# Optimization experiments

Measured on AMD Instinct MI355X. Metric: run time of the kernel, lower is better.

The kernel has to match this reference:

```python
import jax, jax.numpy as jnp
import numpy as np

B, CIN, H, W = 4, 256, 32, 32
COUT, DK, DV, NH = 256, 64, 64, 8
L = H * W
DKH = DK // NH
DVH = DV // NH
ALPHA, BETA = 0.5, 0.5
PAD = 1
LEAK = 0.01
GN_EPS = 1e-5


def conv2d(x, w, b=None, padding=0):
    out = jax.lax.conv_general_dilated(
        x, w, window_strides=(1, 1),
        padding=[(padding, padding), (padding, padding)],
        dimension_numbers=('NCHW', 'OIHW', 'NCHW'))
    if b is not None:
        out = out + b[None, :, None, None]
    return out


def rel_to_abs(x):
    # x: [B, Nh, L, 2L-1] -> [B, Nh, L, L]
    b, nh, l, _ = x.shape
    x = jnp.concatenate([x, jnp.zeros((b, nh, l, 1), x.dtype)], axis=3)
    flat = x.reshape(b, nh, l * 2 * l)
    flat = jnp.concatenate([flat, jnp.zeros((b, nh, l - 1), x.dtype)], axis=2)
    final = flat.reshape(b, nh, l + 1, 2 * l - 1)
    return final[:, :, :l, l - 1:]


def setup_inputs() -> dict:
    key = jax.random.key(0)
    ks = jax.random.split(key, 8)
    s = 0.02
    return {
        'x': jax.random.normal(ks[0], (B, CIN, H, W), jnp.float32),
        'prev_att': jax.random.normal(ks[1], (B, NH, L, L), jnp.float32) * 0.1,
        'conv_v': jax.random.normal(ks[2], (COUT - DV, CIN, 3, 3), jnp.float32) * s,
        'conv_g': jnp.ones((COUT - DV, 1, 1, 1), jnp.float32),
        'conv_b': jnp.zeros((COUT - DV,), jnp.float32),
        'qkv_w': jax.random.normal(ks[3], (2 * DK + DV, CIN, 1, 1), jnp.float32) * s,
        'qkv_b': jnp.zeros((2 * DK + DV,), jnp.float32),
        'attc_w': jax.random.normal(ks[4], (NH, NH, 3, 3), jnp.float32) * s,
        'attc_b': jnp.zeros((NH,), jnp.float32),
        'gn_w': jnp.ones((NH,), jnp.float32),
        'gn_b': jnp.zeros((NH,), jnp.float32),
        'rel_k': jax.random.normal(ks[5], (2 * L - 1, DKH), jnp.float32),
    }


def reference(x, prev_att, conv_v, conv_g, conv_b, qkv_w, qkv_b,
              attc_w, attc_b, gn_w, gn_b, rel_k):
    # ---- weight-normed conv branch (k < 1) ----
    vnorm = jnp.sqrt(jnp.sum(conv_v * conv_v, axis=(1, 2, 3), keepdims=True))
    w_eff = conv_g * conv_v / vnorm
    conv_out = conv2d(x, w_eff, conv_b, padding=PAD)
    conv_out = conv_out[:, :, :-PAD, :-PAD]  # Chomp2d

    # ---- attention branch (dk > 0, no downsample) ----
    qkv = conv2d(x, qkv_w, qkv_b, padding=0).reshape(B, 2 * DK + DV, L)
    q = qkv[:, :DK].reshape(B, NH, DKH, L) * (DKH ** -0.5)
    k = qkv[:, DK:2 * DK].reshape(B, NH, DKH, L)
    v = qkv[:, 2 * DK:].reshape(B, NH, DVH, L)

    logits = jnp.einsum('bhdl,bhdm->bhlm', q, k)  # [B,Nh,L,L]

    # relative position logits
    rel = jnp.einsum('bhld,md->bhlm', q.transpose(0, 1, 3, 2), rel_k)  # [B,Nh,L,2L-1]
    logits = logits + rel_to_abs(rel)

    # blend with previous attention + conv/GroupNorm refinement
    att_matrix = (1.0 - BETA) * logits + BETA * prev_att
    t = conv2d(att_matrix, attc_w, attc_b, padding=1)
    mu = jnp.mean(t, axis=(1, 2, 3), keepdims=True)
    var = jnp.var(t, axis=(1, 2, 3), keepdims=True)
    t = (t - mu) / jnp.sqrt(var + GN_EPS)
    t = t * gn_w[None, :, None, None] + gn_b[None, :, None, None]
    t = jnp.where(t >= 0, t, LEAK * t)  # LeakyReLU
    logits = ALPHA * t + (1.0 - ALPHA) * att_matrix

    weights = jax.nn.softmax(logits, axis=-1)
    attn = jnp.einsum('bhlm,bhmd->bhld', weights, v.transpose(0, 1, 3, 2))  # [B,Nh,L,dvh]
    # faithful to torch: reshape (not transpose) [B,Nh,L,dvh] -> [B,Nh,dvh,L]
    attn = attn.reshape(B, NH, DVH, L).reshape(B, DV, H, W)
    attn = attn[:, :, :-PAD, :-PAD]  # Chomp2d

    out = jnp.concatenate([conv_out, attn], axis=1)  # [B, COUT, H-1, W-1]
    return (out, logits)
```

## Files before the change

kernel.cpp:

```cpp
#include <hip/hip_runtime.h>
#include <math.h>

#define NB   4
#define CINc 256
#define LLEN 1024
#define NHEAD 8
#define QKVOC 192
#define CONVOC 192
#define OHW  31

#define WS_SCALE 0
#define WS_STATS 192
#define WS_PART  256
#define WS_QKV   8448
#define WS_E     794880
#define WS_CPART 1057024

typedef __attribute__((ext_vector_type(8))) short bf16x8;
typedef __attribute__((ext_vector_type(4))) float f32x4;

__device__ __forceinline__ unsigned short f2bf(float f) {
    unsigned int u = __float_as_uint(f);
    u += 0x7FFFu + ((u >> 16) & 1u);
    return (unsigned short)(u >> 16);
}
__device__ __forceinline__ float bf2f(unsigned short s) {
    return __uint_as_float(((unsigned int)s) << 16);
}

__global__ void k_wnorm(const float* __restrict__ conv_v, const float* __restrict__ conv_g,
                        float* __restrict__ ws) {
    int o = blockIdx.x, t = threadIdx.x;
    const float* v = conv_v + (size_t)o * 2304;
    float s = 0.f;
    for (int i = t; i < 2304; i += 256) { float x = v[i]; s += x * x; }
    for (int off = 1; off < 64; off <<= 1) s += __shfl_xor(s, off, 64);
    __shared__ float red[4];
    if ((t & 63) == 0) red[t >> 6] = s;
    __syncthreads();
    if (t == 0) {
        float tot = red[0] + red[1] + red[2] + red[3];
        ws[WS_SCALE + o] = conv_g[o] / sqrtf(tot);
    }
}

__global__ __launch_bounds__(256) void k_qkv(const float* __restrict__ x,
                                             const float* __restrict__ qkv_w,
                                             const float* __restrict__ qkv_b,
                                             float* __restrict__ ws) {
    int og = blockIdx.x, b = blockIdx.y, t = threadIdx.x;
    int o0 = og * 4;
    const float* xb = x + (size_t)b * CINc * LLEN;
    float acc[4][4] = {};
    for (int c = 0; c < CINc; c++) {
        float xv[4];
#pragma unroll
        for (int k = 0; k < 4; k++) xv[k] = xb[(size_t)c * LLEN + t + 256 * k];
#pragma unroll
        for (int oo = 0; oo < 4; oo++) {
            float w = qkv_w[(size_t)(o0 + oo) * CINc + c];
#pragma unroll
            for (int k = 0; k < 4; k++) acc[oo][k] += w * xv[k];
        }
    }
#pragma unroll
    for (int oo = 0; oo < 4; oo++) {
        int o = o0 + oo;
        float bias = qkv_b[o];
        float sc = (o < 64) ? 0.35355339059327373f : 1.0f;
#pragma unroll
        for (int k = 0; k < 4; k++)
            ws[WS_QKV + ((size_t)b * QKVOC + o) * LLEN + t + 256 * k] = (acc[oo][k] + bias) * sc;
    }
}

__global__ __launch_bounds__(256) void k_conv(const float* __restrict__ x,
                                              const float* __restrict__ conv_v,
                                              float* __restrict__ ws) {
    int ot = blockIdx.x, z = blockIdx.y, b = blockIdx.z, t = threadIdx.x;
    int o0 = ot * 4, c0 = z * 32;
    __shared__ float xs[34 * 35];
    __shared__ float wS[32 * 9 * 4];
    for (int idx = t; idx < 1152; idx += 256) {
        int oo = idx & 3, rem = idx >> 2;
        int c = rem / 9, k = rem - c * 9;
        wS[idx] = conv_v[((size_t)(o0 + oo) * CINc + c0 + c) * 9 + k];
    }
    for (int i = t; i < 34 * 35; i += 256) xs[i] = 0.f;
    int h = t >> 3, wq = t & 7, w0 = wq * 4;
    const float* xb = x + ((size_t)b * CINc + c0) * 1024;
    float acc[4][4] = {};
    for (int c = 0; c < 32; c++) {
        __syncthreads();
        {
            int idx4 = t * 4;
            int r = idx4 >> 5, cc = idx4 & 31;
            float4 v = *reinterpret_cast<const float4*>(&xb[(size_t)c * 1024 + idx4]);
            float* dst = &xs[(r + 1) * 35 + cc + 1];
            dst[0] = v.x; dst[1] = v.y; dst[2] = v.z; dst[3] = v.w;
        }
        __syncthreads();
        float wv[3][6];
#pragma unroll
        for (int dr = 0; dr < 3; dr++)
#pragma unroll
            for (int u = 0; u < 6; u++)
                wv[dr][u] = xs[(h + dr) * 35 + w0 + u];
        const float* wp = &wS[c * 36];
#pragma unroll
        for (int dr = 0; dr < 3; dr++)
#pragma unroll
            for (int dc = 0; dc < 3; dc++) {
                float4 w4 = *reinterpret_cast<const float4*>(&wp[(dr * 3 + dc) * 4]);
#pragma unroll
                for (int px = 0; px < 4; px++) {
                    float xv = wv[dr][dc + px];
                    acc[0][px] += w4.x * xv; acc[1][px] += w4.y * xv;
                    acc[2][px] += w4.z * xv; acc[3][px] += w4.w * xv;
                }
            }
    }
#pragma unroll
    for (int oo = 0; oo < 4; oo++) {
        size_t off = WS_CPART + ((size_t)(b * 8 + z) * CONVOC + o0 + oo) * 1024 + t * 4;
        *reinterpret_cast<float4*>(&ws[off]) =
            make_float4(acc[oo][0], acc[oo][1], acc[oo][2], acc[oo][3]);
    }
}

__global__ __launch_bounds__(256) void k_convred(const float* __restrict__ conv_b,
                                                 const float* __restrict__ ws,
                                                 float* __restrict__ out) {
    int o = blockIdx.x, b = blockIdx.y, t = threadIdx.x;
    float sc = ws[WS_SCALE + o], bi = conv_b[o];
    for (int px = t; px < 1024; px += 256) {
        float s = 0.f;
#pragma unroll
        for (int z = 0; z < 8; z++)
            s += ws[WS_CPART + ((size_t)(b * 8 + z) * CONVOC + o) * 1024 + px];
        int hh = px >> 5, ww = px & 31;
        if (hh < 31 && ww < 31)
            out[((size_t)(b * 256 + o) * 31 + hh) * 31 + ww] = sc * s + bi;
    }
}

__global__ __launch_bounds__(256, 3) void k_att(const float* __restrict__ ws_,
                                                const float* __restrict__ prev,
                                                const float* __restrict__ rel_k,
                                                unsigned short* __restrict__ attB) {
    int jt = blockIdx.x, it = blockIdx.y, bh = blockIdx.z;
    int b = bh >> 3, h = bh & 7;
    int t = threadIdx.x;
    int i0 = it * 32, j0 = jt * 128;
    int ig = t >> 5, tj = t & 31;

    float4 pv[4];
    size_t poff = (((size_t)bh * 1024 + i0 + ig * 4) << 10) + j0 + tj * 4;
#pragma unroll
    for (int ii = 0; ii < 4; ii++)
        pv[ii] = *reinterpret_cast<const float4*>(&prev[poff + ((size_t)ii << 10)]);
    const float* rbase = rel_k + (size_t)(j0 - i0 + 1020 + 4 * (tj - ig)) * 8;
    float4 ra[7], rb[7];
#pragma unroll
    for (int dgi = 0; dgi < 7; dgi++) {
        ra[dgi] = *reinterpret_cast<const float4*>(rbase + dgi * 8);
        rb[dgi] = *reinterpret_cast<const float4*>(rbase + dgi * 8 + 4);
    }

    __shared__ float kS[8][128];
    __shared__ float qS[32][8];
    const float* qkv = ws_ + WS_QKV;
    const float* qplane = qkv + ((size_t)b * QKVOC + h * 8) * LLEN;
    const float* kplane = qkv + ((size_t)b * QKVOC + 64 + h * 8) * LLEN;
    {
        int d = t >> 5, jc = (t & 31) * 4;
        *reinterpret_cast<float4*>(&kS[d][jc]) =
            *reinterpret_cast<const float4*>(&kplane[(size_t)d * LLEN + j0 + jc]);
    }
    {
        int i = t >> 3, d = t & 7;
        qS[i][d] = qplane[(size_t)d * LLEN + i0 + i];
    }
    __syncthreads();

    float qr[4][8];
#pragma unroll
    for (int ii = 0; ii < 4; ii++) {
        float4 a = *reinterpret_cast<const float4*>(&qS[ig * 4 + ii][0]);
        float4 c = *reinterpret_cast<const float4*>(&qS[ig * 4 + ii][4]);
        qr[ii][0] = a.x; qr[ii][1] = a.y; qr[ii][2] = a.z; qr[ii][3] = a.w;
        qr[ii][4] = c.x; qr[ii][5] = c.y; qr[ii][6] = c.z; qr[ii][7] = c.w;
    }
    float acc[4][4] = {};
#pragma unroll
    for (int d = 0; d < 8; d++) {
        float4 kv = *reinterpret_cast<const float4*>(&kS[d][tj * 4]);
#pragma unroll
        for (int ii = 0; ii < 4; ii++) {
            float qv = qr[ii][d];
            acc[ii][0] += qv * kv.x; acc[ii][1] += qv * kv.y;
            acc[ii][2] += qv * kv.z; acc[ii][3] += qv * kv.w;
        }
    }
#pragma unroll
    for (int dgi = 0; dgi < 7; dgi++) {
#pragma unroll
        for (int ii = 0; ii < 4; ii++) {
#pragma unroll
            for (int jj = 0; jj < 4; jj++) {
                if (jj - ii + 3 == dgi) {
                    acc[ii][jj] += qr[ii][0] * ra[dgi].x + qr[ii][1] * ra[dgi].y
                                 + qr[ii][2] * ra[dgi].z + qr[ii][3] * ra[dgi].w
                                 + qr[ii][4] * rb[dgi].x + qr[ii][5] * rb[dgi].y
                                 + qr[ii][6] * rb[dgi].z + qr[ii][7] * rb[dgi].w;
                }
            }
        }
    }
#pragma unroll
    for (int ii = 0; ii < 4; ii++) {
        int i = i0 + ig * 4 + ii;
        size_t off = (((size_t)bh * 1024 + i) << 10) + j0 + tj * 4;
        ushort4 o16;
        o16.x = f2bf(0.5f * acc[ii][0] + 0.5f * pv[ii].x);
        o16.y = f2bf(0.5f * acc[ii][1] + 0.5f * pv[ii].y);
        o16.z = f2bf(0.5f * acc[ii][2] + 0.5f * pv[ii].z);
        o16.w = f2bf(0.5f * acc[ii][3] + 0.5f * pv[ii].w);
        *reinterpret_cast<ushort4*>(&attB[off]) = o16;
    }
}

__global__ __launch_bounds__(256) void k_attconv(const unsigned short* __restrict__ attB,
                                                 const float* __restrict__ attc_w,
                                                 const float* __restrict__ attc_b,
                                                 unsigned short* __restrict__ tB,
                                                 float* __restrict__ ws) {
    int jt = blockIdx.x, it = blockIdx.y, b = blockIdx.z, t = threadIdx.x;
    int i0 = it * 16, j0 = jt * 64;
    __shared__ unsigned short aW[16 * 96];
    __shared__ unsigned short xT[18 * 81 * 8];
    unsigned int* xU = reinterpret_cast<unsigned int*>(xT);

    for (int idx = t; idx < 1536; idx += 256) {
        int ho = idx / 96, k = idx - ho * 96;
        int tap = k >> 3, hp = k & 7;
        float w = (ho < 8 && tap < 9) ? attc_w[ho * 72 + hp * 9 + tap] : 0.f;
        aW[ho * 96 + k] = f2bf(w);
    }
    const unsigned short* attb = attB + (((size_t)b * 8) << 20);
    for (int task = t; task < 720; task += 256) {
        int r   = task % 18;
        int hpp = (task / 18) & 3;
        int ch  = task / 72;
        int gr  = i0 - 1 + r;
        int gc0 = j0 - 8 + ch * 8;
        uint4 va = make_uint4(0u, 0u, 0u, 0u), vb = va;
        if (gr >= 0 && gr < 1024 && gc0 >= 0 && gc0 < 1024) {
            size_t base = (((size_t)(hpp * 2)) << 20) + ((size_t)gr << 10) + gc0;
            va = *reinterpret_cast<const uint4*>(&attb[base]);
            vb = *reinterpret_cast<const uint4*>(&attb[base + (1u << 20)]);
        }
        int cbase = (r * 81 + ch * 8) * 4 + hpp;
        unsigned int aw[4] = {va.x, va.y, va.z, va.w};
        unsigned int bw[4] = {vb.x, vb.y, vb.z, vb.w};
#pragma unroll
        for (int q = 0; q < 4; q++) {
            xU[cbase + (2 * q) * 4]     = (aw[q] & 0xffffu) | (bw[q] << 16);
            xU[cbase + (2 * q + 1) * 4] = (aw[q] >> 16) | (bw[q] & 0xffff0000u);
        }
    }
    __syncthreads();

    int lane = t & 63, w = t >> 6;
    int col = lane & 15, kb = lane >> 4;
    bf16x8 afr[3];
#pragma unroll
    for (int c = 0; c < 3; c++)
        afr[c] = *reinterpret_cast<const bf16x8*>(&aW[col * 96 + c * 32 + kb * 8]);
    int offs[3];
#pragma unroll
    for (int c = 0; c < 3; c++) {
        int tap = c * 4 + kb;
        int di = (tap < 9) ? tap / 3 : 1;
        int dj = (tap < 9) ? tap % 3 : 1;
        offs[c] = (di * 81 + col + dj + 7) * 16;
    }
    float bias_r[4];
#pragma unroll
    for (int r = 0; r < 4; r++) {
        int ho = kb * 4 + r;
        bias_r[r] = (ho < 8) ? attc_b[ho] : 0.f;
    }
    float ssum = 0.f, ssq = 0.f;
    char* xbyte = reinterpret_cast<char*>(xT);
#pragma unroll
    for (int ri = 0; ri < 4; ri++) {
        int il = w * 4 + ri;
#pragma unroll
        for (int jg = 0; jg < 4; jg++) {
            f32x4 acc = {0.f, 0.f, 0.f, 0.f};
            int base = (il * 81 + jg * 16) * 16;
#pragma unroll
            for (int c = 0; c < 3; c++) {
                bf16x8 bfr = *reinterpret_cast<const bf16x8*>(xbyte + base + offs[c]);
                acc = __builtin_amdgcn_mfma_f32_16x16x32_bf16(afr[c], bfr, acc, 0, 0, 0);
            }
#pragma unroll
            for (int r = 0; r < 4; r++) {
                float v = acc[r] + bias_r[r];
                ssum += v; ssq += v * v;
                int ho = kb * 4 + r;
                if (ho < 8) {
                    size_t off = (((size_t)(b * 8 + ho)) << 20) + ((size_t)(i0 + il) << 10)
                               + j0 + jg * 16 + col;
                    tB[off] = f2bf(v);
                }
            }
        }
    }
    for (int off = 1; off < 64; off <<= 1) {
        ssum += __shfl_xor(ssum, off, 64);
        ssq  += __shfl_xor(ssq, off, 64);
    }
    __shared__ float r1[4], r2[4];
    if ((t & 63) == 0) { r1[t >> 6] = ssum; r2[t >> 6] = ssq; }
    __syncthreads();
    if (t == 0) {
        int lin = (b * 64 + it) * 16 + jt;
        ws[WS_PART + lin * 2]     = r1[0] + r1[1] + r1[2] + r1[3];
        ws[WS_PART + lin * 2 + 1] = r2[0] + r2[1] + r2[2] + r2[3];
    }
}

__global__ void k_stats(float* __restrict__ ws) {
    int b = blockIdx.x, t = threadIdx.x;
    float S = 0.f, Q = 0.f;
    for (int n = t; n < 1024; n += 256) {
        S += ws[WS_PART + (size_t)(b * 1024 + n) * 2];
        Q += ws[WS_PART + (size_t)(b * 1024 + n) * 2 + 1];
    }
    for (int off = 1; off < 64; off <<= 1) { S += __shfl_xor(S, off, 64); Q += __shfl_xor(Q, off, 64); }
    __shared__ float r1[4], r2[4];
    if ((t & 63) == 0) { r1[t >> 6] = S; r2[t >> 6] = Q; }
    __syncthreads();
    if (t == 0) {
        float Sa = r1[0] + r1[1] + r1[2] + r1[3];
        float Qa = r2[0] + r2[1] + r2[2] + r2[3];
        float N = 8.0f * 1024.f * 1024.f;
        float mean = Sa / N;
        float var = Qa / N - mean * mean;
        ws[WS_STATS + b * 2]     = mean;
        ws[WS_STATS + b * 2 + 1] = 1.0f / sqrtf(var + 1e-5f);
    }
}

__global__ __launch_bounds__(256) void k_final(const unsigned short* __restrict__ tB,
                                               const unsigned short* __restrict__ attB,
                                               float* __restrict__ logits,
                                               const float* __restrict__ gn_w,
                                               const float* __restrict__ gn_b,
                                               float* __restrict__ ws) {
    int row = blockIdx.x;
    int b = row >> 13, h = (row >> 10) & 7;
    int t = threadIdx.x;
    float mean = ws[WS_STATS + b * 2], rstd = ws[WS_STATS + b * 2 + 1];
    float gw = gn_w[h], gb = gn_b[h];
    size_t roff = (size_t)row * 1024 + t * 4;
    ushort4 tv = *reinterpret_cast<const ushort4*>(&tB[roff]);
    ushort4 av = *reinterpret_cast<const ushort4*>(&attB[roff]);
    float lg[4];
    {
        float tt[4] = {bf2f(tv.x), bf2f(tv.y), bf2f(tv.z), bf2f(tv.w)};
        float aa[4] = {bf2f(av.x), bf2f(av.y), bf2f(av.z), bf2f(av.w)};
#pragma unroll
        for (int k = 0; k < 4; k++) {
            float xv = (tt[k] - mean) * rstd * gw + gb;
            xv = (xv >= 0.f) ? xv : 0.01f * xv;
            lg[k] = 0.5f * xv + 0.5f * aa[k];
        }
    }
    *reinterpret_cast<float4*>(&logits[roff]) = make_float4(lg[0], lg[1], lg[2], lg[3]);
    float m = fmaxf(fmaxf(lg[0], lg[1]), fmaxf(lg[2], lg[3]));
    for (int off = 1; off < 64; off <<= 1) m = fmaxf(m, __shfl_xor(m, off, 64));
    __shared__ float red[4], red2[4];
    __shared__ float p[1024];
    int wvi = t >> 6, ln = t & 63;
    if (ln == 0) red[wvi] = m;
    __syncthreads();
    m = fmaxf(fmaxf(red[0], red[1]), fmaxf(red[2], red[3]));
    float e[4]; float s = 0.f;
#pragma unroll
    for (int k = 0; k < 4; k++) { e[k] = __expf(lg[k] - m); s += e[k]; }
    *reinterpret_cast<float4*>(&p[t * 4]) = make_float4(e[0], e[1], e[2], e[3]);
    for (int off = 1; off < 64; off <<= 1) s += __shfl_xor(s, off, 64);
    if (ln == 0) red2[wvi] = s;
    __syncthreads();
    s = red2[0] + red2[1] + red2[2] + red2[3];
    int d = t >> 5, c = t & 31;
    const float* vrow = ws + WS_QKV + ((size_t)b * QKVOC + 128 + h * 8 + d) * LLEN;
    float a = 0.f;
#pragma unroll
    for (int u = 0; u < 8; u++) {
        int j = 4 * c + 128 * u;
        float4 pv = *reinterpret_cast<const float4*>(&p[j]);
        float4 vv = *reinterpret_cast<const float4*>(&vrow[j]);
        a += pv.x * vv.x + pv.y * vv.y + pv.z * vv.z + pv.w * vv.w;
    }
#pragma unroll
    for (int off = 1; off < 32; off <<= 1) a += __shfl_xor(a, off, 64);
    if (c == 0)
        ws[WS_E + (size_t)row * 8 + d] = a / s;
}

__global__ void k_scatter(const float* __restrict__ ws, float* __restrict__ out) {
    int idx = blockIdx.x * 256 + threadIdx.x;
    if (idx >= 4 * 64 * 31 * 31) return;
    int x = idx % 31; int rest = idx / 31;
    int y = rest % 31; rest /= 31;
    int hd = rest % 64; int b = rest / 64;
    int h = hd >> 3, d = hd & 7;
    int flat = d * 1024 + y * 32 + x;
    int lp = flat >> 3, mp = flat & 7;
    float v = ws[WS_E + ((size_t)(b * 8 + h) * 1024 + lp) * 8 + mp];
    out[((size_t)(b * 256 + 192 + hd) * 31 + y) * 31 + x] = v;
}

extern "C" void kernel_launch(void* const* d_in, const int* in_sizes, int n_in,
                              void* d_out, int out_size, void* d_ws, size_t ws_size,
                              hipStream_t stream) {
    (void)in_sizes; (void)n_in; (void)out_size; (void)ws_size;
    const float* x      = (const float*)d_in[0];
    const float* prev   = (const float*)d_in[1];
    const float* conv_v = (const float*)d_in[2];
    const float* conv_g = (const float*)d_in[3];
    const float* conv_b = (const float*)d_in[4];
    const float* qkv_w  = (const float*)d_in[5];
    const float* qkv_b  = (const float*)d_in[6];
    const float* attc_w = (const float*)d_in[7];
    const float* attc_b = (const float*)d_in[8];
    const float* gn_w   = (const float*)d_in[9];
    const float* gn_b   = (const float*)d_in[10];
    const float* rel_k  = (const float*)d_in[11];
    float* out = (float*)d_out;
    float* ws  = (float*)d_ws;
    float* logits = out + 984064;
    unsigned short* attB = (unsigned short*)(ws + 1057024);
    unsigned short* tB   = attB + 33554432;

    k_wnorm<<<192, 256, 0, stream>>>(conv_v, conv_g, ws);
    k_qkv<<<dim3(48, 4), 256, 0, stream>>>(x, qkv_w, qkv_b, ws);
    k_conv<<<dim3(48, 8, 4), 256, 0, stream>>>(x, conv_v, ws);
    k_convred<<<dim3(192, 4), 256, 0, stream>>>(conv_b, ws, out);
    k_att<<<dim3(8, 32, 32), 256, 0, stream>>>(ws, prev, rel_k, attB);
    k_attconv<<<dim3(16, 64, 4), 256, 0, stream>>>(attB, attc_w, attc_b, tB, ws);
    k_stats<<<4, 256, 0, stream>>>(ws);
    k_final<<<32768, 256, 0, stream>>>(tB, attB, logits, gn_w, gn_b, ws);
    k_scatter<<<961, 256, 0, stream>>>(ws, out);
}
```

Before: 300.5 us.

## Rewrite 3x3 weight-normed conv as implicit GEMM on bf16 MFMA

The 3x3 conv kernel now runs as an implicit GEMM on MFMA 16x16x32 bf16 instructions instead of scalar FP32 FMAs. Weights and a padded, channel-interleaved input tile for half the image are converted to bf16 in shared memory, and each wave computes 16 output channels by 16 pixels per tile across the 9 taps. This cuts the compute cost of the conv branch. In exchange it lowers precision to bf16 inputs and changes the grid to 16 output channels per block with the image split into two row halves.

```diff
diff --git a/kernel.cpp b/kernel.cpp
--- a/kernel.cpp
+++ b/kernel.cpp
@@ -77,54 +77,67 @@
 __global__ __launch_bounds__(256) void k_conv(const float* __restrict__ x,
                                               const float* __restrict__ conv_v,
                                               float* __restrict__ ws) {
-    int ot = blockIdx.x, z = blockIdx.y, b = blockIdx.z, t = threadIdx.x;
-    int o0 = ot * 4, c0 = z * 32;
-    __shared__ float xs[34 * 35];
-    __shared__ float wS[32 * 9 * 4];
-    for (int idx = t; idx < 1152; idx += 256) {
-        int oo = idx & 3, rem = idx >> 2;
-        int c = rem / 9, k = rem - c * 9;
-        wS[idx] = conv_v[((size_t)(o0 + oo) * CINc + c0 + c) * 9 + k];
-    }
-    for (int i = t; i < 34 * 35; i += 256) xs[i] = 0.f;
-    int h = t >> 3, wq = t & 7, w0 = wq * 4;
+    int ot = blockIdx.x, z = blockIdx.y, bz = blockIdx.z, t = threadIdx.x;
+    int b = bz >> 1, half = bz & 1;
+    int o0 = ot * 16, c0 = z * 32, r0 = half * 16;
+    __shared__ unsigned short aW[16 * 288];
+    __shared__ unsigned short xS[18 * 34 * 36];
+
+    for (int idx = t; idx < 4608; idx += 256) {
+        int o = idx / 288, k = idx - o * 288;
+        int tap = k >> 5, c = k & 31;
+        aW[o * 288 + k] = f2bf(conv_v[((size_t)(o0 + o) * CINc + c0 + c) * 9 + tap]);
+    }
+    unsigned int* xSu = reinterpret_cast<unsigned int*>(xS);
+    for (int i = t; i < 11016; i += 256) xSu[i] = 0u;
+    __syncthreads();
     const float* xb = x + ((size_t)b * CINc + c0) * 1024;
-    float acc[4][4] = {};
-    for (int c = 0; c < 32; c++) {
-        __syncthreads();
-        {
-            int idx4 = t * 4;
-            int r = idx4 >> 5, cc = idx4 & 31;
-            float4 v = *reinterpret_cast<const float4*>(&xb[(size_t)c * 1024 + idx4]);
-            float* dst = &xs[(r + 1) * 35 + cc + 1];
-            dst[0] = v.x; dst[1] = v.y; dst[2] = v.z; dst[3] = v.w;
-        }
-        __syncthreads();
-        float wv[3][6];
-#pragma unroll
-        for (int dr = 0; dr < 3; dr++)
-#pragma unroll
-            for (int u = 0; u < 6; u++)
-                wv[dr][u] = xs[(h + dr) * 35 + w0 + u];
-        const float* wp = &wS[c * 36];
-#pragma unroll
-        for (int dr = 0; dr < 3; dr++)
-#pragma unroll
-            for (int dc = 0; dc < 3; dc++) {
-                float4 w4 = *reinterpret_cast<const float4*>(&wp[(dr * 3 + dc) * 4]);
-#pragma unroll
-                for (int px = 0; px < 4; px++) {
-                    float xv = wv[dr][dc + px];
-                    acc[0][px] += w4.x * xv; acc[1][px] += w4.y * xv;
-                    acc[2][px] += w4.z * xv; acc[3][px] += w4.w * xv;
-                }
+    for (int task = t; task < 2304; task += 256) {
+        int cp = task & 15;
+        int rr = (task >> 4) % 18;
+        int wc = task / 288;
+        int gr = r0 - 1 + rr;
+        int gw = wc * 4;
+        if (gr >= 0 && gr < 32) {
+            float4 va = *reinterpret_cast<const float4*>(&xb[(size_t)(2 * cp) * 1024 + gr * 32 + gw]);
+            float4 vb = *reinterpret_cast<const float4*>(&xb[(size_t)(2 * cp + 1) * 1024 + gr * 32 + gw]);
+            int base = (rr * 34 + gw + 1) * 36 + 2 * cp;
+            float a0[4] = {va.x, va.y, va.z, va.w};
+            float b0[4] = {vb.x, vb.y, vb.z, vb.w};
+#pragma unroll
+            for (int j = 0; j < 4; j++) {
+                unsigned int pk = (unsigned int)f2bf(a0[j]) | ((unsigned int)f2bf(b0[j]) << 16);
+                *reinterpret_cast<unsigned int*>(&xS[base + j * 36]) = pk;
             }
-    }
-#pragma unroll
-    for (int oo = 0; oo < 4; oo++) {
-        size_t off = WS_CPART + ((size_t)(b * 8 + z) * CONVOC + o0 + oo) * 1024 + t * 4;
-        *reinterpret_cast<float4*>(&ws[off]) =
-            make_float4(acc[oo][0], acc[oo][1], acc[oo][2], acc[oo][3]);
+        }
+    }
+    __syncthreads();
+
+    int lane = t & 63, w = t >> 6;
+    int col = lane & 15, kb = lane >> 4;
+    bf16x8 afr[9];
+#pragma unroll
+    for (int tap = 0; tap < 9; tap++)
+        afr[tap] = *reinterpret_cast<const bf16x8*>(&aW[col * 288 + tap * 32 + kb * 8]);
+    char* xb8 = reinterpret_cast<char*>(xS);
+#pragma unroll
+    for (int tt = 0; tt < 8; tt++) {
+        int pt = w * 8 + tt;
+        int hl = pt >> 1, w0 = (pt & 1) * 16;
+        f32x4 acc = {0.f, 0.f, 0.f, 0.f};
+        int pbase = (hl * 34 + w0 + col) * 72 + kb * 16;
+#pragma unroll
+        for (int tap = 0; tap < 9; tap++) {
+            int di = tap / 3, dj = tap % 3;
+            bf16x8 bfr = *reinterpret_cast<const bf16x8*>(xb8 + pbase + (di * 34 + dj) * 72);
+            acc = __builtin_amdgcn_mfma_f32_16x16x32_bf16(afr[tap], bfr, acc, 0, 0, 0);
+        }
+        int px = (r0 + hl) * 32 + w0 + col;
+#pragma unroll
+        for (int r = 0; r < 4; r++) {
+            int o = kb * 4 + r;
+            ws[WS_CPART + ((size_t)(b * 8 + z) * CONVOC + o0 + o) * 1024 + px] = acc[r];
+        }
     }
 }
 
@@ -449,7 +462,7 @@
 
     k_wnorm<<<192, 256, 0, stream>>>(conv_v, conv_g, ws);
     k_qkv<<<dim3(48, 4), 256, 0, stream>>>(x, qkv_w, qkv_b, ws);
-    k_conv<<<dim3(48, 8, 4), 256, 0, stream>>>(x, conv_v, ws);
+    k_conv<<<dim3(12, 8, 8), 256, 0, stream>>>(x, conv_v, ws);
     k_convred<<<dim3(192, 4), 256, 0, stream>>>(conv_b, ws, out);
     k_att<<<dim3(8, 32, 32), 256, 0, stream>>>(ws, prev, rel_k, attB);
     k_attconv<<<dim3(16, 64, 4), 256, 0, stream>>>(attB, attc_w, attc_b, tB, ws);
```

New measurement: 293.3 us. 2.4% less time.
